# Optimization experiments

Measured on AMD Instinct MI355X. Metric: run time of the kernel, lower is better.

## Reference

```python
import jax, jax.numpy as jnp
import numpy as np

BIG_NUMBER = 1e7   # repo constant used to mask padded adjacency slots
MAX_ITERS = 32     # params['flow_iters']


def _build_graph(B, N, D, valid_deg, seed=0):
    """Random d-regular-ish graph: each valid slot d holds a permutation of nodes,
    so every node has exactly `valid_deg` in-edges. in_indices[b,v,d] = (b,u,s)
    such that adj[b,u,s] == v. Padded slots (d >= valid_deg) hold the sentinel N
    and their in_indices point to a padded (near-zero-weight) flow entry."""
    rng = np.random.default_rng(seed)
    adj = np.full((B, N, D), N, dtype=np.int32)
    in_idx = np.zeros((B, N, D, 3), dtype=np.int32)
    in_idx[..., 0] = np.arange(B, dtype=np.int32)[:, None, None]
    in_idx[..., 2] = valid_deg  # padded slots -> flow[b, 0, valid_deg] (weight ~ 0)
    for b in range(B):
        for d in range(valid_deg):
            perm = rng.permutation(N).astype(np.int32)
            adj[b, :, d] = perm                      # edge u -> perm[u] via slot d
            inv = np.argsort(perm).astype(np.int32)  # inv[v] = u with perm[u] == v
            in_idx[b, :, d, 1] = inv
            in_idx[b, :, d, 2] = d
    return jnp.asarray(adj), jnp.asarray(in_idx)


def setup_inputs():
    B, N, D, VALID = 4, 100000, 16, 12
    key = jax.random.key(0)
    k1, k2 = jax.random.split(key)
    adj_lst, in_indices = _build_graph(B, N, D, VALID)
    return {
        "flow_proportions": jax.random.normal(k1, (B, N, D), dtype=jnp.float32),
        "demands": jax.random.normal(k2, (B, N, 1), dtype=jnp.float32),
        "adj_lst": adj_lst,
        "in_indices": in_indices,
        "num_nodes": N,
    }


def reference(flow_proportions, demands, adj_lst, in_indices, num_nodes):
    # --- masked softmax over neighbor slots (padded slots get -BIG_NUMBER) ---
    mask = (adj_lst == num_nodes).astype(flow_proportions.dtype)   # [B,N,D]
    masked = flow_proportions - BIG_NUMBER * mask
    weights = jax.nn.softmax(masked, axis=-1)                      # normalized_weights

    # --- mcf_solver: iterate flow <- weights * relu(inflow - demand) ---
    bidx = in_indices[..., 0]   # [B,N,D] batch index
    src = in_indices[..., 1]    # [B,N,D] source node of d-th in-edge
    slot = in_indices[..., 2]   # [B,N,D] slot of this node in source's adj list

    def step(flow, _):
        # gather incoming edge flows, sum -> inflow per node [B,N,1]
        inflow = flow[bidx, src, slot].sum(axis=-1, keepdims=True)
        new_flow = weights * jax.nn.relu(inflow - demands)
        return new_flow, None

    flow, _ = jax.lax.scan(step, jnp.zeros_like(weights), None, length=MAX_ITERS)
    # flow_cost (loss) = sum over nodes/slots of cost_fn(flow) = flow**2 here:
    # flow_cost = jnp.sum(flow * flow, axis=(1, 2))
    return flow
```

## Files before the change

kernel.cpp:

```cpp
#include <hip/hip_runtime.h>

#define DEG 16
#define MAX_ITERS 32

__global__ void softmax_k(const float* __restrict__ fp, const int* __restrict__ adj,
                          const int* __restrict__ nn, float* __restrict__ wout,
                          int nodes) {
    int i = blockIdx.x * blockDim.x + threadIdx.x;
    if (i >= nodes) return;
    const int N = *nn;
    const size_t base = (size_t)i * DEG;
    const float4* f4 = (const float4*)(fp + base);
    const int4*   a4 = (const int4*)(adj + base);
    float v[DEG];
#pragma unroll
    for (int k = 0; k < DEG / 4; ++k) {
        float4 f = f4[k];
        int4   a = a4[k];
        v[4*k+0] = (a.x == N) ? f.x - 1e7f : f.x;
        v[4*k+1] = (a.y == N) ? f.y - 1e7f : f.y;
        v[4*k+2] = (a.z == N) ? f.z - 1e7f : f.z;
        v[4*k+3] = (a.w == N) ? f.w - 1e7f : f.w;
    }
    float m = v[0];
#pragma unroll
    for (int j = 1; j < DEG; ++j) m = fmaxf(m, v[j]);
    float s = 0.f;
#pragma unroll
    for (int j = 0; j < DEG; ++j) { v[j] = expf(v[j] - m); s += v[j]; }
    float inv = 1.f / s;
    float4* w4 = (float4*)(wout + base);
#pragma unroll
    for (int k = 0; k < DEG / 4; ++k) {
        float4 o;
        o.x = v[4*k+0] * inv;
        o.y = v[4*k+1] * inv;
        o.z = v[4*k+2] * inv;
        o.w = v[4*k+3] * inv;
        w4[k] = o;
    }
}

__global__ void gather_k(const int* __restrict__ in_idx, const float* __restrict__ w,
                         const int* __restrict__ nn, int* __restrict__ e_src,
                         float* __restrict__ e_w, int edges) {
    int e = blockIdx.x * blockDim.x + threadIdx.x;
    if (e >= edges) return;
    const int N = *nn;
    size_t e3 = 3 * (size_t)e;
    int b  = in_idx[e3 + 0];
    int s  = in_idx[e3 + 1];
    int sl = in_idx[e3 + 2];
    int fi = b * N + s;
    e_src[e] = fi;
    e_w[e]   = w[(size_t)fi * DEG + sl];
}

__global__ void iter_k(const int* __restrict__ e_src, const float* __restrict__ e_w,
                       const float* __restrict__ dem, const float* __restrict__ Rin,
                       float* __restrict__ Rout, int nodes) {
    int i = blockIdx.x * blockDim.x + threadIdx.x;
    if (i >= nodes) return;
    const size_t base = (size_t)i * DEG;
    const int4*   s4 = (const int4*)(e_src + base);
    const float4* w4 = (const float4*)(e_w + base);
    float acc = 0.f;
#pragma unroll
    for (int k = 0; k < DEG / 4; ++k) {
        int4   s = s4[k];
        float4 w = w4[k];
        acc += w.x * Rin[s.x];
        acc += w.y * Rin[s.y];
        acc += w.z * Rin[s.z];
        acc += w.w * Rin[s.w];
    }
    float r = acc - dem[i];
    Rout[i] = r > 0.f ? r : 0.f;
}

__global__ void final_k(const float* __restrict__ w, const float* __restrict__ R,
                        float* __restrict__ out, int nodes) {
    int i = blockIdx.x * blockDim.x + threadIdx.x;
    if (i >= nodes) return;
    float r = R[i];
    const size_t base = (size_t)i * DEG;
    const float4* w4 = (const float4*)(w + base);
    float4* o4 = (float4*)(out + base);
#pragma unroll
    for (int k = 0; k < DEG / 4; ++k) {
        float4 v = w4[k];
        v.x *= r; v.y *= r; v.z *= r; v.w *= r;
        o4[k] = v;
    }
}

extern "C" void kernel_launch(void* const* d_in, const int* in_sizes, int n_in,
                              void* d_out, int out_size, void* d_ws, size_t ws_size,
                              hipStream_t stream) {
    const float* fp  = (const float*)d_in[0];
    const float* dem = (const float*)d_in[1];
    const int*   adj = (const int*)d_in[2];
    const int*   idx = (const int*)d_in[3];
    const int*   nn  = (const int*)d_in[4];

    const int edges = in_sizes[0];
    const int nodes = in_sizes[1];

    float* weights = (float*)d_out;

    char* ws = (char*)d_ws;
    int*   e_src = (int*)ws;   ws += (size_t)edges * sizeof(int);
    float* e_w   = (float*)ws; ws += (size_t)edges * sizeof(float);
    float* R0    = (float*)ws; ws += (size_t)nodes * sizeof(float);
    float* R1    = (float*)ws;

    hipMemsetAsync(R0, 0, (size_t)nodes * sizeof(float), stream);

    const int blk = 256;
    const int gn = (nodes + blk - 1) / blk;
    const int ge = (edges + blk - 1) / blk;

    softmax_k<<<gn, blk, 0, stream>>>(fp, adj, nn, weights, nodes);
    gather_k<<<ge, blk, 0, stream>>>(idx, weights, nn, e_src, e_w, edges);

    float* a = R0;
    float* b = R1;
    for (int t = 0; t < MAX_ITERS; ++t) {
        iter_k<<<gn, blk, 0, stream>>>(e_src, e_w, dem, a, b, nodes);
        float* tmp = a; a = b; b = tmp;
    }

    final_k<<<gn, blk, 0, stream>>>(weights, a, (float*)d_out, nodes);
}
```

Measured before the change: 1.028 ms.

## Fuse softmax, gather and all iterations into one cooperative persistent kernel

Replaces the chain of roughly 35 kernel launches with a single cooperative kernel that uses grid-wide syncs between phases and iterations. Each thread keeps its 16 in-edge source indices and weights in registers, so the per-iteration reloads of e_src/e_w are gone. The first iteration is computed analytically from the zero start, and the memset is dropped. The kernel also switches to the fast __expf. It falls back to the multi-launch path when the grid (1563 blocks of 256) cannot be fully co-resident; that needs about 7 blocks per CU on 256 CUs, which launch_bounds(256,7) targets. Grid syncs on large grids can be costly.

```diff
diff --git a/kernel.cpp b/kernel.cpp
--- a/kernel.cpp
+++ b/kernel.cpp
@@ -1,7 +1,106 @@
 #include <hip/hip_runtime.h>
+#include <hip/hip_cooperative_groups.h>
+
+namespace cg = cooperative_groups;
 
 #define DEG 16
 #define MAX_ITERS 32
+
+__global__ __launch_bounds__(256, 7)
+void fused_k(const float* __restrict__ fp, const int* __restrict__ adj,
+             const int* __restrict__ in_idx, const float* __restrict__ dem,
+             const int* __restrict__ nn, float* __restrict__ wout,
+             float* __restrict__ Ra, float* __restrict__ Rb, int nodes) {
+    cg::grid_group grid = cg::this_grid();
+    const int i = blockIdx.x * blockDim.x + threadIdx.x;
+    const bool act = (i < nodes);
+    const int N = *nn;
+    const size_t base = (size_t)i * DEG;
+
+    if (act) {
+        const float4* f4 = (const float4*)(fp + base);
+        const int4*   a4 = (const int4*)(adj + base);
+        float v[DEG];
+#pragma unroll
+        for (int k = 0; k < DEG / 4; ++k) {
+            float4 f = f4[k];
+            int4   a = a4[k];
+            v[4*k+0] = (a.x == N) ? f.x - 1e7f : f.x;
+            v[4*k+1] = (a.y == N) ? f.y - 1e7f : f.y;
+            v[4*k+2] = (a.z == N) ? f.z - 1e7f : f.z;
+            v[4*k+3] = (a.w == N) ? f.w - 1e7f : f.w;
+        }
+        float m = v[0];
+#pragma unroll
+        for (int j = 1; j < DEG; ++j) m = fmaxf(m, v[j]);
+        float s = 0.f;
+#pragma unroll
+        for (int j = 0; j < DEG; ++j) { v[j] = __expf(v[j] - m); s += v[j]; }
+        float inv = 1.f / s;
+        float4* w4 = (float4*)(wout + base);
+#pragma unroll
+        for (int k = 0; k < DEG / 4; ++k) {
+            float4 o;
+            o.x = v[4*k+0] * inv;
+            o.y = v[4*k+1] * inv;
+            o.z = v[4*k+2] * inv;
+            o.w = v[4*k+3] * inv;
+            w4[k] = o;
+        }
+    }
+    __threadfence();
+    grid.sync();
+
+    int   src[DEG];
+    float w[DEG];
+    float dval = 0.f;
+    if (act) {
+        dval = dem[i];
+        const int* t = in_idx + 3 * base;
+#pragma unroll
+        for (int k = 0; k < DEG; ++k) {
+            int b  = t[3*k + 0];
+            int s  = t[3*k + 1];
+            int sl = t[3*k + 2];
+            int fi = b * N + s;
+            src[k] = fi;
+            w[k]   = wout[(size_t)fi * DEG + sl];
+        }
+    } else {
+#pragma unroll
+        for (int k = 0; k < DEG; ++k) { src[k] = 0; w[k] = 0.f; }
+    }
+
+    float r = fmaxf(-dval, 0.f);
+    if (act) Ra[i] = r;
+    __threadfence();
+    grid.sync();
+
+    float* Rin  = Ra;
+    float* Rout = Rb;
+    for (int t = 1; t < MAX_ITERS; ++t) {
+        if (act) {
+            float acc = 0.f;
+#pragma unroll
+            for (int k = 0; k < DEG; ++k) acc += w[k] * Rin[src[k]];
+            r = fmaxf(acc - dval, 0.f);
+            Rout[i] = r;
+        }
+        __threadfence();
+        grid.sync();
+        float* tmp = Rin; Rin = Rout; Rout = tmp;
+    }
+
+    if (act) {
+        float4* w4 = (float4*)(wout + base);
+#pragma unroll
+        for (int k = 0; k < DEG / 4; ++k) {
+            float4 v = w4[k];
+            v.x *= r; v.y *= r; v.z *= r; v.w *= r;
+            w4[k] = v;
+        }
+    }
+}
 
 __global__ void softmax_k(const float* __restrict__ fp, const int* __restrict__ adj,
                           const int* __restrict__ nn, float* __restrict__ wout,
@@ -27,7 +126,7 @@
     for (int j = 1; j < DEG; ++j) m = fmaxf(m, v[j]);
     float s = 0.f;
 #pragma unroll
-    for (int j = 0; j < DEG; ++j) { v[j] = expf(v[j] - m); s += v[j]; }
+    for (int j = 0; j < DEG; ++j) { v[j] = __expf(v[j] - m); s += v[j]; }
     float inv = 1.f / s;
     float4* w4 = (float4*)(wout + base);
 #pragma unroll
@@ -114,21 +213,31 @@
     float* R0    = (float*)ws; ws += (size_t)nodes * sizeof(float);
     float* R1    = (float*)ws;
 
-    hipMemsetAsync(R0, 0, (size_t)nodes * sizeof(float), stream);
-
     const int blk = 256;
     const int gn = (nodes + blk - 1) / blk;
     const int ge = (edges + blk - 1) / blk;
 
-    softmax_k<<<gn, blk, 0, stream>>>(fp, adj, nn, weights, nodes);
-    gather_k<<<ge, blk, 0, stream>>>(idx, weights, nn, e_src, e_w, edges);
-
-    float* a = R0;
-    float* b = R1;
-    for (int t = 0; t < MAX_ITERS; ++t) {
-        iter_k<<<gn, blk, 0, stream>>>(e_src, e_w, dem, a, b, nodes);
-        float* tmp = a; a = b; b = tmp;
-    }
-
-    final_k<<<gn, blk, 0, stream>>>(weights, a, (float*)d_out, nodes);
-}
+    int dev = 0, cus = 0, maxBlk = 0;
+    hipGetDevice(&dev);
+    hipDeviceGetAttribute(&cus, hipDeviceAttributeMultiprocessorCount, dev);
+    hipOccupancyMaxActiveBlocksPerMultiprocessor(&maxBlk, (const void*)fused_k, blk, 0);
+
+    if ((long long)maxBlk * cus >= gn) {
+        void* args[] = { (void*)&fp, (void*)&adj, (void*)&idx, (void*)&dem,
+                         (void*)&nn, (void*)&weights, (void*)&R0, (void*)&R1,
+                         (void*)&nodes };
+        hipLaunchCooperativeKernel((const void*)fused_k, dim3(gn), dim3(blk),
+                                   args, 0, stream);
+    } else {
+        hipMemsetAsync(R0, 0, (size_t)nodes * sizeof(float), stream);
+        softmax_k<<<gn, blk, 0, stream>>>(fp, adj, nn, weights, nodes);
+        gather_k<<<ge, blk, 0, stream>>>(idx, weights, nn, e_src, e_w, edges);
+        float* a = R0;
+        float* b = R1;
+        for (int t = 0; t < MAX_ITERS; ++t) {
+            iter_k<<<gn, blk, 0, stream>>>(e_src, e_w, dem, a, b, nodes);
+            float* tmp = a; a = b; b = tmp;
+        }
+        final_k<<<gn, blk, 0, stream>>>(weights, a, (float*)d_out, nodes);
+    }
+}
```

Measured after the change: 1.027 ms. Within noise of the previous version (-0.1%).

## Fuse softmax, gather and all flow iterations into one cooperative persistent kernel

Applied to the files above, without the earlier changes.

Replaces the chain of per-iteration kernel launches with a single cooperative kernel that uses a software grid barrier between phases. Each thread handles two nodes and keeps their edge sources and weights in registers across all iterations. It also skips edge slots whose weights are zero across the whole wave, computes the first iteration analytically, and uses fast __expf. The intent is to remove launch overhead and the repeated reloading of edge arrays. In exchange it adds grid-wide atomic barrier costs and higher register pressure, and it falls back to the old multi-kernel path when occupancy is insufficient.

```diff
diff --git a/kernel.cpp b/kernel.cpp
--- a/kernel.cpp
+++ b/kernel.cpp
@@ -2,14 +2,33 @@
 
 #define DEG 16
 #define MAX_ITERS 32
-
-__global__ void softmax_k(const float* __restrict__ fp, const int* __restrict__ adj,
-                          const int* __restrict__ nn, float* __restrict__ wout,
-                          int nodes) {
-    int i = blockIdx.x * blockDim.x + threadIdx.x;
-    if (i >= nodes) return;
-    const int N = *nn;
-    const size_t base = (size_t)i * DEG;
+#define BLK_F 1024
+
+__device__ __forceinline__ void grid_barrier(unsigned* cnt, unsigned* gen,
+                                             unsigned target, unsigned nblocks) {
+    __syncthreads();
+    if (threadIdx.x == 0) {
+        __threadfence();
+        unsigned arrived = __hip_atomic_fetch_add(cnt, 1u, __ATOMIC_ACQ_REL,
+                                                  __HIP_MEMORY_SCOPE_AGENT);
+        if (arrived == nblocks - 1u) {
+            __hip_atomic_store(cnt, 0u, __ATOMIC_RELAXED, __HIP_MEMORY_SCOPE_AGENT);
+            __hip_atomic_fetch_add(gen, 1u, __ATOMIC_RELEASE, __HIP_MEMORY_SCOPE_AGENT);
+        } else {
+            while (__hip_atomic_load(gen, __ATOMIC_RELAXED,
+                                     __HIP_MEMORY_SCOPE_AGENT) < target) {
+                __builtin_amdgcn_s_sleep(16);
+            }
+        }
+        __threadfence();
+    }
+    __syncthreads();
+}
+
+__device__ __forceinline__ void softmax_row(const float* __restrict__ fp,
+                                            const int* __restrict__ adj,
+                                            float* __restrict__ wout,
+                                            size_t base, int N) {
     const float4* f4 = (const float4*)(fp + base);
     const int4*   a4 = (const int4*)(adj + base);
     float v[DEG];
@@ -27,7 +46,7 @@
     for (int j = 1; j < DEG; ++j) m = fmaxf(m, v[j]);
     float s = 0.f;
 #pragma unroll
-    for (int j = 0; j < DEG; ++j) { v[j] = expf(v[j] - m); s += v[j]; }
+    for (int j = 0; j < DEG; ++j) { v[j] = __expf(v[j] - m); s += v[j]; }
     float inv = 1.f / s;
     float4* w4 = (float4*)(wout + base);
 #pragma unroll
@@ -39,6 +58,117 @@
         o.w = v[4*k+3] * inv;
         w4[k] = o;
     }
+}
+
+__global__ __launch_bounds__(BLK_F, 4)
+void fused2_k(const float* __restrict__ fp, const int* __restrict__ adj,
+              const int* __restrict__ in_idx, const float* __restrict__ dem,
+              const int* __restrict__ nn, float* __restrict__ wout,
+              float* __restrict__ Ra, float* __restrict__ Rb,
+              unsigned* __restrict__ bar_cnt, unsigned* __restrict__ bar_gen,
+              int nodes) {
+    const int tid = blockIdx.x * blockDim.x + threadIdx.x;
+    const int T = gridDim.x * blockDim.x;
+    const int N = *nn;
+    const unsigned nb = gridDim.x;
+    unsigned bar = 0;
+
+    const int  n0 = tid, n1 = tid + T;
+    const bool a0 = (n0 < nodes), a1 = (n1 < nodes);
+    const size_t b0 = (size_t)n0 * DEG, b1 = (size_t)n1 * DEG;
+
+    if (a0) softmax_row(fp, adj, wout, b0, N);
+    if (a1) softmax_row(fp, adj, wout, b1, N);
+    grid_barrier(bar_cnt, bar_gen, ++bar, nb);
+
+    int   src0[DEG], src1[DEG];
+    float w0[DEG],   w1[DEG];
+    float d0 = 0.f, d1 = 0.f;
+    unsigned skipA = 0, skipB = 0;
+    if (a0) {
+        d0 = dem[n0];
+        const int* t = in_idx + 3 * b0;
+#pragma unroll
+        for (int k = 0; k < DEG; ++k) {
+            int fi = t[3*k] * N + t[3*k + 1];
+            src0[k] = fi;
+            w0[k]   = wout[(size_t)fi * DEG + t[3*k + 2]];
+        }
+    } else {
+#pragma unroll
+        for (int k = 0; k < DEG; ++k) { src0[k] = 0; w0[k] = 0.f; }
+    }
+    if (a1) {
+        d1 = dem[n1];
+        const int* t = in_idx + 3 * b1;
+#pragma unroll
+        for (int k = 0; k < DEG; ++k) {
+            int fi = t[3*k] * N + t[3*k + 1];
+            src1[k] = fi;
+            w1[k]   = wout[(size_t)fi * DEG + t[3*k + 2]];
+        }
+    } else {
+#pragma unroll
+        for (int k = 0; k < DEG; ++k) { src1[k] = 0; w1[k] = 0.f; }
+    }
+#pragma unroll
+    for (int k = 0; k < DEG; ++k) {
+        if (__ballot(w0[k] != 0.f) == 0ull) skipA |= (1u << k);
+        if (__ballot(w1[k] != 0.f) == 0ull) skipB |= (1u << k);
+    }
+    const unsigned sk0 = __builtin_amdgcn_readfirstlane(skipA);
+    const unsigned sk1 = __builtin_amdgcn_readfirstlane(skipB);
+
+    float r0 = fmaxf(-d0, 0.f), r1 = fmaxf(-d1, 0.f);
+    if (a0) Ra[n0] = r0;
+    if (a1) Ra[n1] = r1;
+    grid_barrier(bar_cnt, bar_gen, ++bar, nb);
+
+    const float* Rin = Ra;
+    float*       Rout = Rb;
+    for (int t = 1; t < MAX_ITERS; ++t) {
+        float acc0 = 0.f, acc1 = 0.f;
+#pragma unroll
+        for (int k = 0; k < DEG; ++k) {
+            if (!((sk0 >> k) & 1u) && a0) acc0 += w0[k] * Rin[src0[k]];
+            if (!((sk1 >> k) & 1u) && a1) acc1 += w1[k] * Rin[src1[k]];
+        }
+        r0 = fmaxf(acc0 - d0, 0.f);
+        r1 = fmaxf(acc1 - d1, 0.f);
+        if (t < MAX_ITERS - 1) {
+            if (a0) Rout[n0] = r0;
+            if (a1) Rout[n1] = r1;
+            grid_barrier(bar_cnt, bar_gen, ++bar, nb);
+            float* tmp = (float*)Rin; Rin = Rout; Rout = tmp;
+        }
+    }
+
+    if (a0) {
+        float4* w4 = (float4*)(wout + b0);
+#pragma unroll
+        for (int k = 0; k < DEG / 4; ++k) {
+            float4 v = w4[k];
+            v.x *= r0; v.y *= r0; v.z *= r0; v.w *= r0;
+            w4[k] = v;
+        }
+    }
+    if (a1) {
+        float4* w4 = (float4*)(wout + b1);
+#pragma unroll
+        for (int k = 0; k < DEG / 4; ++k) {
+            float4 v = w4[k];
+            v.x *= r1; v.y *= r1; v.z *= r1; v.w *= r1;
+            w4[k] = v;
+        }
+    }
+}
+
+__global__ void softmax_k(const float* __restrict__ fp, const int* __restrict__ adj,
+                          const int* __restrict__ nn, float* __restrict__ wout,
+                          int nodes) {
+    int i = blockIdx.x * blockDim.x + threadIdx.x;
+    if (i >= nodes) return;
+    softmax_row(fp, adj, wout, (size_t)i * DEG, *nn);
 }
 
 __global__ void gather_k(const int* __restrict__ in_idx, const float* __restrict__ w,
@@ -48,12 +178,9 @@
     if (e >= edges) return;
     const int N = *nn;
     size_t e3 = 3 * (size_t)e;
-    int b  = in_idx[e3 + 0];
-    int s  = in_idx[e3 + 1];
-    int sl = in_idx[e3 + 2];
-    int fi = b * N + s;
+    int fi = in_idx[e3] * N + in_idx[e3 + 1];
     e_src[e] = fi;
-    e_w[e]   = w[(size_t)fi * DEG + sl];
+    e_w[e]   = w[(size_t)fi * DEG + in_idx[e3 + 2]];
 }
 
 __global__ void iter_k(const int* __restrict__ e_src, const float* __restrict__ e_w,
@@ -109,26 +236,42 @@
     float* weights = (float*)d_out;
 
     char* ws = (char*)d_ws;
-    int*   e_src = (int*)ws;   ws += (size_t)edges * sizeof(int);
-    float* e_w   = (float*)ws; ws += (size_t)edges * sizeof(float);
-    float* R0    = (float*)ws; ws += (size_t)nodes * sizeof(float);
-    float* R1    = (float*)ws;
-
-    hipMemsetAsync(R0, 0, (size_t)nodes * sizeof(float), stream);
-
-    const int blk = 256;
-    const int gn = (nodes + blk - 1) / blk;
-    const int ge = (edges + blk - 1) / blk;
-
-    softmax_k<<<gn, blk, 0, stream>>>(fp, adj, nn, weights, nodes);
-    gather_k<<<ge, blk, 0, stream>>>(idx, weights, nn, e_src, e_w, edges);
-
-    float* a = R0;
-    float* b = R1;
-    for (int t = 0; t < MAX_ITERS; ++t) {
-        iter_k<<<gn, blk, 0, stream>>>(e_src, e_w, dem, a, b, nodes);
-        float* tmp = a; a = b; b = tmp;
-    }
-
-    final_k<<<gn, blk, 0, stream>>>(weights, a, (float*)d_out, nodes);
-}
+    unsigned* bar_cnt = (unsigned*)ws;
+    unsigned* bar_gen = (unsigned*)(ws + 128);
+    int*   e_src = (int*)ws;
+    float* e_w   = (float*)(ws + (size_t)edges * sizeof(int));
+    float* R0    = (float*)(ws + (size_t)edges * sizeof(int) + (size_t)edges * sizeof(float));
+    float* R1    = R0 + nodes;
+
+    const int threads_needed = (nodes + 1) / 2;
+    const int gf = (threads_needed + BLK_F - 1) / BLK_F;
+
+    int dev = 0, cus = 0, maxBlk = 0;
+    hipGetDevice(&dev);
+    hipDeviceGetAttribute(&cus, hipDeviceAttributeMultiprocessorCount, dev);
+    hipOccupancyMaxActiveBlocksPerMultiprocessor(&maxBlk, (const void*)fused2_k,
+                                                 BLK_F, 0);
+
+    if ((long long)maxBlk * cus >= gf) {
+        hipMemsetAsync(ws, 0, 256, stream);
+        void* args[] = { (void*)&fp, (void*)&adj, (void*)&idx, (void*)&dem,
+                         (void*)&nn, (void*)&weights, (void*)&R0, (void*)&R1,
+                         (void*)&bar_cnt, (void*)&bar_gen, (void*)&nodes };
+        hipLaunchCooperativeKernel((const void*)fused2_k, dim3(gf), dim3(BLK_F),
+                                   args, 0, stream);
+    } else {
+        const int blk = 256;
+        const int gn = (nodes + blk - 1) / blk;
+        const int ge = (edges + blk - 1) / blk;
+        hipMemsetAsync(R0, 0, (size_t)nodes * sizeof(float), stream);
+        softmax_k<<<gn, blk, 0, stream>>>(fp, adj, nn, weights, nodes);
+        gather_k<<<ge, blk, 0, stream>>>(idx, weights, nn, e_src, e_w, edges);
+        float* a = R0;
+        float* b = R1;
+        for (int t = 0; t < MAX_ITERS; ++t) {
+            iter_k<<<gn, blk, 0, stream>>>(e_src, e_w, dem, a, b, nodes);
+            float* tmp = a; a = b; b = tmp;
+        }
+        final_k<<<gn, blk, 0, stream>>>(weights, a, (float*)d_out, nodes);
+    }
+}
```

Result: no change. 1.028 ms (-0.0%).
